# Performance work log

Hardware: AMD Instinct MI355X
Metric: run time of the kernel (lower is better)

The kernel has to match this reference:

```python
import jax, jax.numpy as jnp
import numpy as np

WS = 4        # window_size
SHIFT = 2     # shift
NHEADS = 8


def setup_inputs():
    key = jax.random.key(0)
    k = jax.random.split(key, 5)
    N, C, H, W = 16, 512, 96, 96
    x = jax.random.normal(k[0], (N, C, H, W), dtype=jnp.float32)
    # nn.MultiheadAttention parameters
    in_proj_w = jax.random.normal(k[1], (3 * C, C), dtype=jnp.float32) * 0.02
    in_proj_b = jax.random.normal(k[2], (3 * C,), dtype=jnp.float32) * 0.02
    out_w = jax.random.normal(k[3], (C, C), dtype=jnp.float32) * 0.02
    out_b = jax.random.normal(k[4], (C,), dtype=jnp.float32) * 0.02
    return {"x": x, "in_proj_w": in_proj_w, "in_proj_b": in_proj_b,
            "out_w": out_w, "out_b": out_b}


def _split_window(x, ws):
    # replicates torch: cat(split(x, ws, dim=3), dim=2); cat(split(x, ws, dim=2), dim=0)
    N, C, Hp, Wp = x.shape
    nh, nw = Hp // ws, Wp // ws
    x = x.reshape(N, C, nh, ws, nw, ws)      # n c ib wi jb wj
    x = x.transpose(4, 2, 0, 1, 3, 5)        # jb ib n c wi wj (col-block outermost in batch)
    return x.reshape(nw * nh * N, C, ws, ws), nh, nw


def _concat_window(x, nh, nw, ws):
    # inverse of _split_window, replicating torch chunk/cat order
    N = x.shape[0] // (nh * nw)
    C = x.shape[1]
    x = x.reshape(nw, nh, N, C, ws, ws)      # jb ib n c wi wj
    x = x.transpose(2, 3, 1, 4, 0, 5)        # n c ib wi jb wj
    return x.reshape(N, C, nh * ws, nw * ws)


def _mha(xt, mask_f, in_proj_w, in_proj_b, out_w, out_b):
    # xt: (B, L, C); mask_f: (B, L) FLOAT key_padding_mask -> added to logits (torch semantics)
    B, L, C = xt.shape
    d = C // NHEADS
    qkv = xt @ in_proj_w.T + in_proj_b                     # (B, L, 3C)
    q, k, v = jnp.split(qkv, 3, axis=-1)
    heads = lambda t: t.reshape(B, L, NHEADS, d).transpose(0, 2, 1, 3)  # (B, H, L, d)
    q, k, v = heads(q), heads(k), heads(v)
    scale = float(1.0 / np.sqrt(d))
    scores = jnp.einsum('bhqd,bhkd->bhqk', q, k) * scale
    scores = scores + mask_f[:, None, None, :]             # additive float key mask
    attn = jax.nn.softmax(scores, axis=-1)
    o = jnp.einsum('bhqk,bhkd->bhqd', attn, v)
    o = o.transpose(0, 2, 1, 3).reshape(B, L, C)
    return o @ out_w.T + out_b


def reference(x, in_proj_w, in_proj_b, out_w, out_b):
    N, C, H, W = x.shape
    ws = WS
    pad_h, pad_w = ws - H % ws, ws - W % ws   # note: pads a full window even when divisible
    x = jnp.pad(x, ((0, 0), (0, 0), (0, pad_h), (0, pad_w)))
    x = jnp.roll(x, (SHIFT, SHIFT), axis=(2, 3))
    # BUG-FAITHFUL: source overwrites the boolean mask with a second roll of x,
    # so the "mask" is the doubly-rolled float feature map.
    mask = jnp.roll(x, (SHIFT, SHIFT), axis=(2, 3))
    xw, nh, nw = _split_window(x, ws)
    mw, _, _ = _split_window(mask, ws)
    B = xw.shape[0]
    xt = xw.reshape(B, C, ws * ws).transpose(0, 2, 1)      # (B, L=ws*ws, C)
    mask_f = mw[:, 0].reshape(B, ws * ws)                  # channel-0 float "mask"
    ot = _mha(xt, mask_f, in_proj_w, in_proj_b, out_w, out_b)
    ow = ot.transpose(0, 2, 1).reshape(B, C, ws, ws)
    out = _concat_window(ow, nh, nw, ws)
    out = jnp.roll(out, (-SHIFT, -SHIFT), axis=(2, 3))
    return out[:, :, :H, :W]
```

## Files before the change

kernel.cpp:

```cpp
#include <hip/hip_runtime.h>
#include <cstdint>


typedef __attribute__((ext_vector_type(8))) __bf16 bf16x8;
typedef __attribute__((ext_vector_type(8))) uint16_t u16x8;
typedef __attribute__((ext_vector_type(4))) float f32x4;

__device__ __forceinline__ uint16_t f2bf(float f) {
  union { float f; uint32_t u; } c; c.f = f;
  uint32_t r = c.u + 0x7FFFu + ((c.u >> 16) & 1u);
  return (uint16_t)(r >> 16);
}
__device__ __forceinline__ float bf2f(uint16_t u) {
  union { uint32_t u; float f; } c; c.u = ((uint32_t)u) << 16;
  return c.f;
}

__device__ __forceinline__ void g2lds16(const void* g, void* lds) {
  __builtin_amdgcn_global_load_lds(
      (const __attribute__((address_space(1))) uint32_t*)(uintptr_t)g,
      (__attribute__((address_space(3))) uint32_t*)(uintptr_t)lds,
      16, 0, 0);
}

#define CFENCE asm volatile("" ::: "memory")
#define BAR do { CFENCE; __builtin_amdgcn_s_barrier(); CFENCE; } while (0)

__global__ void cvt_weights(const float* __restrict__ w1, const float* __restrict__ w2,
                            uint16_t* __restrict__ o1, uint16_t* __restrict__ o2) {
  int i = blockIdx.x * 256 + threadIdx.x;
  if (i < 786432) o1[i] = f2bf(w1[i]);
  if (i < 262144) o2[i] = f2bf(w2[i]);
}

__global__ __launch_bounds__(256) void gather_kernel(
    const float* __restrict__ x, uint16_t* __restrict__ xbf, int n0) {
  __shared__ float tile[64][65];
  const int z = blockIdx.z;
  const int g = z / 100, hh = z % 100;
  const int c0 = blockIdx.y * 64, ww0 = blockIdx.x * 64;
  const int n = n0 + g;
  const int hp = (hh >= 2) ? hh - 2 : hh + 98;
  const bool hok = hp < 96;
  const int t = threadIdx.x;
  const int lane = t & 63, grp = t >> 6;

  const int ww = ww0 + lane;
  const int wp = (ww >= 2) ? ww - 2 : ww + 98;
  const bool wok = hok && (ww < 100) && (wp < 96);
  const float* xb = x + ((size_t)n * 512) * 9216 + (size_t)hp * 96 + wp;
#pragma unroll
  for (int i = 0; i < 16; ++i) {
    int c = grp + i * 4;
    tile[c][lane] = wok ? xb[(size_t)(c0 + c) * 9216] : 0.f;
  }
  __syncthreads();
#pragma unroll
  for (int i = 0; i < 16; ++i) {
    int wl = grp + i * 4;
    int www = ww0 + wl;
    if (www < 100) {
      int m = g * 10000 + hh * 100 + www;
      xbf[(size_t)m * 512 + c0 + lane] = f2bf(tile[lane][wl]);
    }
  }
}

template <int EPI, int NB, int MODE>
__global__ __launch_bounds__(512, 2) void gemm8(
    const uint16_t* __restrict__ A, const uint16_t* __restrict__ B,
    const float* __restrict__ bias, uint16_t* __restrict__ Cbf,
    float* __restrict__ Cout, int Mg, int n0) {
  __shared__ alignas(16) uint16_t lds[65536];
  const int t = threadIdx.x;
  const int w = t >> 6, lane = t & 63;
  const int wr = w >> 2, wc = w & 3;
  const int lr = lane & 15, lg = lane >> 4;

  const int nwg = gridDim.x, bid = blockIdx.x;
  const int q = nwg >> 3, r = nwg & 7;
  const int xc = bid & 7, li = bid >> 3;
  const int wg = (xc < r ? xc * (q + 1) : r * (q + 1) + (xc - r) * q) + li;
  int bm, bn;
  if (MODE == 0) { bm = wg / NB; bn = wg % NB; }
  else           { bm = wg % NB; bn = wg / NB; }

  auto STAGE = [&](int kt, int h) {
    const uint16_t* src = (h < 2) ? A : B;
    const int row0 = ((h < 2) ? bm * 256 : bn * 256) + (h & 1) * 128;
    const int base = ((h < 2) ? 0 : 32768) + (kt & 1) * 16384 + (h & 1) * 8192;
#pragma unroll
    for (int i = 0; i < 2; ++i) {
      int e = i * 512 + t;
      int row = e >> 3, slot = e & 7;
      const uint16_t* g = src + (size_t)(row0 + row) * 512 + kt * 64 +
                          ((slot ^ (row & 7)) << 3);
      g2lds16(g, &lds[base + ((i * 512 + w * 64) << 3)]);
    }
  };
  auto LDA = [&](int cur, int mi, int k2) -> bf16x8 {
    int row = wr * 128 + mi * 16 + lr;
    int byte = cur * 32768 + row * 128 + (((k2 * 32 + lg * 8) * 2) ^ ((row & 7) << 4));
    return *(const bf16x8*)((const char*)lds + byte);
  };
  auto LDB = [&](int cur, int ni, int k2) -> bf16x8 {
    int row = wc * 64 + ni * 16 + lr;
    int byte = 65536 + cur * 32768 + row * 128 +
               (((k2 * 32 + lg * 8) * 2) ^ ((row & 7) << 4));
    return *(const bf16x8*)((const char*)lds + byte);
  };

  f32x4 acc[8][4];
#pragma unroll
  for (int mi = 0; mi < 8; ++mi)
#pragma unroll
    for (int ni = 0; ni < 4; ++ni) acc[mi][ni] = (f32x4){0.f, 0.f, 0.f, 0.f};

  STAGE(0, 0); STAGE(0, 1); STAGE(0, 2); STAGE(0, 3);
  STAGE(1, 0); STAGE(1, 1);
  asm volatile("s_waitcnt vmcnt(4)" ::: "memory");
  BAR;

#define MFMAQ(AF, BF, MIOFF, NIOFF)                                        \
  __builtin_amdgcn_s_setprio(1);                                           \
  _Pragma("unroll") for (int mi = 0; mi < 4; ++mi)                         \
  _Pragma("unroll") for (int ni = 0; ni < 2; ++ni)                         \
  _Pragma("unroll") for (int k2 = 0; k2 < 2; ++k2)                         \
      acc[mi + MIOFF][ni + NIOFF] = __builtin_amdgcn_mfma_f32_16x16x32_bf16( \
          AF[mi][k2], BF[ni][k2], acc[mi + MIOFF][ni + NIOFF], 0, 0, 0);   \
  __builtin_amdgcn_s_setprio(0);

  for (int j = 0; j < 8; ++j) {
    const int cur = j & 1;
    bf16x8 a0[4][2], a1[4][2], b0[2][2], b1[2][2];
#pragma unroll
    for (int mi = 0; mi < 4; ++mi)
#pragma unroll
      for (int k2 = 0; k2 < 2; ++k2) a0[mi][k2] = LDA(cur, mi, k2);
#pragma unroll
    for (int ni = 0; ni < 2; ++ni)
#pragma unroll
      for (int k2 = 0; k2 < 2; ++k2) b0[ni][k2] = LDB(cur, ni, k2);
    if (j + 1 < 8) STAGE(j + 1, 2);
    BAR;
    __builtin_amdgcn_sched_barrier(0);
    MFMAQ(a0, b0, 0, 0);
    BAR;
#pragma unroll
    for (int mi = 0; mi < 4; ++mi)
#pragma unroll
      for (int k2 = 0; k2 < 2; ++k2) a1[mi][k2] = LDA(cur, mi + 4, k2);
#pragma unroll
    for (int ni = 0; ni < 2; ++ni)
#pragma unroll
      for (int k2 = 0; k2 < 2; ++k2) b1[ni][k2] = LDB(cur, ni + 2, k2);
    if (j + 1 < 8) STAGE(j + 1, 3);
    BAR;
    __builtin_amdgcn_sched_barrier(0);
    MFMAQ(a1, b1, 4, 2);
    BAR;
    if (j + 2 < 8) STAGE(j + 2, 0);
    BAR;
    __builtin_amdgcn_sched_barrier(0);
    MFMAQ(a0, b1, 0, 2);
    BAR;
    if (j + 2 < 8) STAGE(j + 2, 1);
    if (j < 6) { asm volatile("s_waitcnt vmcnt(4)" ::: "memory"); }
    else       { asm volatile("s_waitcnt vmcnt(0)" ::: "memory"); }
    BAR;
    __builtin_amdgcn_sched_barrier(0);
    MFMAQ(a1, b0, 4, 0);
    BAR;
  }
#undef MFMAQ

  if (EPI == 0) {
#pragma unroll
    for (int ni = 0; ni < 4; ++ni) {
      int col = bn * 256 + wc * 64 + ni * 16 + lr;
      float bb = bias[col];
#pragma unroll
      for (int mi = 0; mi < 8; ++mi) {
        int row = bm * 256 + wr * 128 + mi * 16 + lg * 4;
#pragma unroll
        for (int rr = 0; rr < 4; ++rr)
          Cbf[(size_t)(row + rr) * 1536 + col] = f2bf(acc[mi][ni][rr] + bb);
      }
    }
  } else {
#pragma unroll
    for (int ni = 0; ni < 4; ++ni) {
      int tok = bn * 256 + wc * 64 + ni * 16 + lr;
      if (tok < Mg) {
        int g = tok / 10000, rem = tok % 10000;
        int hh = rem / 100, ww = rem % 100;
        if (hh >= 2 && hh < 98 && ww >= 2 && ww < 98) {
          size_t base = ((size_t)(n0 + g) * 512) * 9216 + (size_t)(hh - 2) * 96 + (ww - 2);
#pragma unroll
          for (int mi = 0; mi < 8; ++mi) {
            int c = bm * 256 + wr * 128 + mi * 16 + lg * 4;
#pragma unroll
            for (int rr = 0; rr < 4; ++rr)
              Cout[base + (size_t)(c + rr) * 9216] = acc[mi][ni][rr] + bias[c + rr];
          }
        }
      }
    }
  }
}

__global__ __launch_bounds__(128) void attn_kernel(
    const uint16_t* __restrict__ qkv, const float* __restrict__ x,
    uint16_t* __restrict__ obuf, int n0) {
  __shared__ alignas(16) uint16_t sq[16][1536];
  __shared__ float smask[16];
  const int b = blockIdx.x;
  const int g = b / 625, wid = b % 625;
  const int ib = wid / 25, jb = wid % 25;
  const int t = threadIdx.x;
  const int mbase = g * 10000 + ib * 400 + jb * 4;

#pragma unroll
  for (int it = 0; it < 24; ++it) {
    int e = it * 128 + t;
    int l = e / 192;
    int off = (e - l * 192) * 8;
    int m = mbase + (l >> 2) * 100 + (l & 3);
    *(uint4*)&sq[l][off] = *(const uint4*)&qkv[(size_t)m * 1536 + off];
  }
  if (t < 16) {
    int hh = ib * 4 + (t >> 2), ww = jb * 4 + (t & 3);
    int a = (hh >= 4) ? hh - 4 : hh + 96;
    int c = (ww >= 4) ? ww - 4 : ww + 96;
    smask[t] = (a < 96 && c < 96)
                   ? x[((size_t)(n0 + g) * 512) * 9216 + (size_t)a * 96 + c]
                   : 0.f;
  }
  __syncthreads();

  const int h = t >> 4, qi = t & 15;
  float qv[64];
#pragma unroll
  for (int d8 = 0; d8 < 8; ++d8) {
    u16x8 v = *(const u16x8*)&sq[qi][h * 64 + d8 * 8];
#pragma unroll
    for (int j = 0; j < 8; ++j) qv[d8 * 8 + j] = bf2f(v[j]);
  }
  float s[16];
  float mx = -1e30f;
#pragma unroll
  for (int ki = 0; ki < 16; ++ki) {
    float a = 0.f;
#pragma unroll
    for (int d8 = 0; d8 < 8; ++d8) {
      u16x8 kv = *(const u16x8*)&sq[ki][512 + h * 64 + d8 * 8];
#pragma unroll
      for (int j = 0; j < 8; ++j) a += qv[d8 * 8 + j] * bf2f(kv[j]);
    }
    s[ki] = a * 0.125f + smask[ki];
    mx = fmaxf(mx, s[ki]);
  }
  float sum = 0.f;
#pragma unroll
  for (int ki = 0; ki < 16; ++ki) { s[ki] = __expf(s[ki] - mx); sum += s[ki]; }
  const float inv = 1.f / sum;
  float o[64];
#pragma unroll
  for (int d = 0; d < 64; ++d) o[d] = 0.f;
#pragma unroll
  for (int ki = 0; ki < 16; ++ki) {
    float wgt = s[ki] * inv;
#pragma unroll
    for (int d8 = 0; d8 < 8; ++d8) {
      u16x8 vv = *(const u16x8*)&sq[ki][1024 + h * 64 + d8 * 8];
#pragma unroll
      for (int j = 0; j < 8; ++j) o[d8 * 8 + j] += wgt * bf2f(vv[j]);
    }
  }
  const int m = mbase + (qi >> 2) * 100 + (qi & 3);
#pragma unroll
  for (int d8 = 0; d8 < 8; ++d8) {
    alignas(16) uint16_t tmp[8];
#pragma unroll
    for (int j = 0; j < 8; ++j) tmp[j] = f2bf(o[d8 * 8 + j]);
    *(uint4*)&obuf[(size_t)m * 512 + h * 64 + d8 * 8] = *(uint4*)tmp;
  }
}

extern "C" void kernel_launch(void* const* d_in, const int* in_sizes, int n_in,
                              void* d_out, int out_size, void* d_ws, size_t ws_size,
                              hipStream_t stream) {
  const float* x  = (const float*)d_in[0];
  const float* wq = (const float*)d_in[1];
  const float* bq = (const float*)d_in[2];
  const float* wo = (const float*)d_in[3];
  const float* bo = (const float*)d_in[4];
  float* out = (float*)d_out;
  uint8_t* ws = (uint8_t*)d_ws;

  uint16_t* wq_bf = (uint16_t*)ws;
  uint16_t* wo_bf = (uint16_t*)(ws + 1572864);
  uint8_t* bufbase = ws + 2097152;

  int G = 16;
  while (G > 1) {
    int Mg = G * 10000;
    int Mp = ((Mg + 255) / 256) * 256;
    size_t need = (size_t)2097152 + (size_t)Mp * 4096;
    if (need <= ws_size) break;
    G >>= 1;
  }
  const int Mg = G * 10000;
  const int Mp = ((Mg + 255) / 256) * 256;
  uint16_t* xo   = (uint16_t*)bufbase;
  uint16_t* qkvb = (uint16_t*)(bufbase + (size_t)Mp * 1024);

  cvt_weights<<<dim3(3072), dim3(256), 0, stream>>>(wq, wo, wq_bf, wo_bf);

  for (int n0 = 0; n0 < 16; n0 += G) {
    gather_kernel<<<dim3(2, 8, G * 100), dim3(256), 0, stream>>>(x, xo, n0);
    gemm8<0, 6, 0><<<dim3((Mp / 256) * 6), dim3(512), 0, stream>>>(
        xo, wq_bf, bq, qkvb, nullptr, Mg, n0);
    attn_kernel<<<dim3(G * 625), dim3(128), 0, stream>>>(qkvb, x, xo, n0);
    gemm8<1, 2, 1><<<dim3((Mp / 256) * 2), dim3(512), 0, stream>>>(
        wo_bf, xo, bo, nullptr, out, Mg, n0);
  }
  (void)in_sizes; (void)n_in; (void)out_size;
}
```

Baseline: 1.063 ms.

## Reorder tokens window-major, stage GEMM epilogues through LDS, prefetch A fragments

Tokens are now laid out window-contiguous (16 tokens per window), so the attention kernel reads contiguous rows and loads K/V into LDS with direct global-to-LDS copies. Q is read straight from global memory. Both GEMM epilogues now stage results through LDS so global stores are vectorised and coalesced; the output-projection epilogue writes float2 runs into NCHW. The GEMM main loop is reordered to prefetch the next tile's A fragments early, and the MFMA operands are swapped for the QKV GEMM. The batch group size drops from 16 to 2, which adds more kernel launches but uses a smaller workspace that may stay resident in cache.

```diff
diff --git a/kernel.cpp b/kernel.cpp
--- a/kernel.cpp
+++ b/kernel.cpp
@@ -25,6 +25,7 @@
 
 #define CFENCE asm volatile("" ::: "memory")
 #define BAR do { CFENCE; __builtin_amdgcn_s_barrier(); CFENCE; } while (0)
+#define SCHED0 __builtin_amdgcn_sched_barrier(0)
 
 __global__ void cvt_weights(const float* __restrict__ w1, const float* __restrict__ w2,
                             uint16_t* __restrict__ o1, uint16_t* __restrict__ o2) {
@@ -60,7 +61,7 @@
     int wl = grp + i * 4;
     int www = ww0 + wl;
     if (www < 100) {
-      int m = g * 10000 + hh * 100 + www;
+      int m = (g * 625 + (hh >> 2) * 25 + (www >> 2)) * 16 + (hh & 3) * 4 + (www & 3);
       xbf[(size_t)m * 512 + c0 + lane] = f2bf(tile[lane][wl]);
     }
   }
@@ -93,9 +94,9 @@
     for (int i = 0; i < 2; ++i) {
       int e = i * 512 + t;
       int row = e >> 3, slot = e & 7;
-      const uint16_t* g = src + (size_t)(row0 + row) * 512 + kt * 64 +
-                          ((slot ^ (row & 7)) << 3);
-      g2lds16(g, &lds[base + ((i * 512 + w * 64) << 3)]);
+      const uint16_t* gp = src + (size_t)(row0 + row) * 512 + kt * 64 +
+                           ((slot ^ (row & 7)) << 3);
+      g2lds16(gp, &lds[base + ((i * 512 + w * 64) << 3)]);
     }
   };
   auto LDA = [&](int cur, int mi, int k2) -> bf16x8 {
@@ -109,6 +110,10 @@
                (((k2 * 32 + lg * 8) * 2) ^ ((row & 7) << 4));
     return *(const bf16x8*)((const char*)lds + byte);
   };
+  auto MM = [&](bf16x8 av, bf16x8 bv, f32x4 c) -> f32x4 {
+    if constexpr (EPI == 0) return __builtin_amdgcn_mfma_f32_16x16x32_bf16(bv, av, c, 0, 0, 0);
+    else                    return __builtin_amdgcn_mfma_f32_16x16x32_bf16(av, bv, c, 0, 0, 0);
+  };
 
   f32x4 acc[8][4];
 #pragma unroll
@@ -121,90 +126,140 @@
   asm volatile("s_waitcnt vmcnt(4)" ::: "memory");
   BAR;
 
-#define MFMAQ(AF, BF, MIOFF, NIOFF)                                        \
-  __builtin_amdgcn_s_setprio(1);                                           \
-  _Pragma("unroll") for (int mi = 0; mi < 4; ++mi)                         \
-  _Pragma("unroll") for (int ni = 0; ni < 2; ++ni)                         \
-  _Pragma("unroll") for (int k2 = 0; k2 < 2; ++k2)                         \
-      acc[mi + MIOFF][ni + NIOFF] = __builtin_amdgcn_mfma_f32_16x16x32_bf16( \
-          AF[mi][k2], BF[ni][k2], acc[mi + MIOFF][ni + NIOFF], 0, 0, 0);   \
+  bf16x8 a0[4][2], a1[4][2], b0[2][2], b1[2][2];
+#pragma unroll
+  for (int mi = 0; mi < 4; ++mi)
+#pragma unroll
+    for (int k2 = 0; k2 < 2; ++k2) a0[mi][k2] = LDA(0, mi, k2);
+
+#define MQUAD(AF, BF, MIOFF, NIOFF)                                         \
+  __builtin_amdgcn_s_setprio(1);                                            \
+  _Pragma("unroll") for (int mi = 0; mi < 4; ++mi)                          \
+  _Pragma("unroll") for (int ni = 0; ni < 2; ++ni)                          \
+  _Pragma("unroll") for (int k2 = 0; k2 < 2; ++k2)                          \
+      acc[mi + MIOFF][ni + NIOFF] =                                         \
+          MM(AF[mi][k2], BF[ni][k2], acc[mi + MIOFF][ni + NIOFF]);          \
   __builtin_amdgcn_s_setprio(0);
 
   for (int j = 0; j < 8; ++j) {
-    const int cur = j & 1;
-    bf16x8 a0[4][2], a1[4][2], b0[2][2], b1[2][2];
+    const int cur = j & 1, nxt = cur ^ 1;
+#pragma unroll
+    for (int ni = 0; ni < 2; ++ni)
+#pragma unroll
+      for (int k2 = 0; k2 < 2; ++k2) b0[ni][k2] = LDB(cur, ni, k2);
 #pragma unroll
     for (int mi = 0; mi < 4; ++mi)
 #pragma unroll
-      for (int k2 = 0; k2 < 2; ++k2) a0[mi][k2] = LDA(cur, mi, k2);
+      for (int k2 = 0; k2 < 2; ++k2) a1[mi][k2] = LDA(cur, mi + 4, k2);
 #pragma unroll
     for (int ni = 0; ni < 2; ++ni)
 #pragma unroll
-      for (int k2 = 0; k2 < 2; ++k2) b0[ni][k2] = LDB(cur, ni, k2);
+      for (int k2 = 0; k2 < 2; ++k2) b1[ni][k2] = LDB(cur, ni + 2, k2);
     if (j + 1 < 8) STAGE(j + 1, 2);
-    BAR;
-    __builtin_amdgcn_sched_barrier(0);
-    MFMAQ(a0, b0, 0, 0);
-    BAR;
-#pragma unroll
-    for (int mi = 0; mi < 4; ++mi)
-#pragma unroll
-      for (int k2 = 0; k2 < 2; ++k2) a1[mi][k2] = LDA(cur, mi + 4, k2);
-#pragma unroll
-    for (int ni = 0; ni < 2; ++ni)
-#pragma unroll
-      for (int k2 = 0; k2 < 2; ++k2) b1[ni][k2] = LDB(cur, ni + 2, k2);
+    BAR; SCHED0;
+    MQUAD(a0, b0, 0, 0);
+    BAR;
     if (j + 1 < 8) STAGE(j + 1, 3);
-    BAR;
-    __builtin_amdgcn_sched_barrier(0);
-    MFMAQ(a1, b1, 4, 2);
+    BAR; SCHED0;
+    MQUAD(a1, b1, 4, 2);
     BAR;
     if (j + 2 < 8) STAGE(j + 2, 0);
-    BAR;
-    __builtin_amdgcn_sched_barrier(0);
-    MFMAQ(a0, b1, 0, 2);
+    BAR; SCHED0;
+    MQUAD(a0, b1, 0, 2);
     BAR;
     if (j + 2 < 8) STAGE(j + 2, 1);
     if (j < 6) { asm volatile("s_waitcnt vmcnt(4)" ::: "memory"); }
     else       { asm volatile("s_waitcnt vmcnt(0)" ::: "memory"); }
     BAR;
-    __builtin_amdgcn_sched_barrier(0);
-    MFMAQ(a1, b0, 4, 0);
-    BAR;
-  }
-#undef MFMAQ
+    if (j + 1 < 8) {
+#pragma unroll
+      for (int mi = 0; mi < 4; ++mi)
+#pragma unroll
+        for (int k2 = 0; k2 < 2; ++k2) a0[mi][k2] = LDA(nxt, mi, k2);
+    }
+    SCHED0;
+    MQUAD(a1, b0, 4, 0);
+    BAR;
+  }
+#undef MQUAD
+
+  __syncthreads();
 
   if (EPI == 0) {
-#pragma unroll
-    for (int ni = 0; ni < 4; ++ni) {
-      int col = bn * 256 + wc * 64 + ni * 16 + lr;
-      float bb = bias[col];
-#pragma unroll
-      for (int mi = 0; mi < 8; ++mi) {
-        int row = bm * 256 + wr * 128 + mi * 16 + lg * 4;
-#pragma unroll
-        for (int rr = 0; rr < 4; ++rr)
-          Cbf[(size_t)(row + rr) * 1536 + col] = f2bf(acc[mi][ni][rr] + bb);
+    uint16_t* ldsE = lds;
+#pragma unroll
+    for (int p = 0; p < 2; ++p) {
+      if (wr == p) {
+#pragma unroll
+        for (int mi = 0; mi < 8; ++mi)
+#pragma unroll
+          for (int ni = 0; ni < 4; ++ni) {
+            const float* b4 = &bias[bn * 256 + wc * 64 + ni * 16 + lg * 4];
+            uint16_t pk[4];
+#pragma unroll
+            for (int rr = 0; rr < 4; ++rr) pk[rr] = f2bf(acc[mi][ni][rr] + b4[rr]);
+            uint2 v; v.x = (uint32_t)pk[0] | ((uint32_t)pk[1] << 16);
+            v.y = (uint32_t)pk[2] | ((uint32_t)pk[3] << 16);
+            *(uint2*)&ldsE[(mi * 16 + lr) * 264 + wc * 64 + ni * 16 + lg * 4] = v;
+          }
       }
+      __syncthreads();
+#pragma unroll
+      for (int i = 0; i < 8; ++i) {
+        int e = i * 512 + t;
+        int mrow = e >> 5, ch = e & 31;
+        int m = bm * 256 + p * 128 + mrow;
+        *(uint4*)&Cbf[(size_t)m * 1536 + bn * 256 + ch * 8] =
+            *(const uint4*)&ldsE[mrow * 264 + ch * 8];
+      }
+      __syncthreads();
     }
   } else {
-#pragma unroll
-    for (int ni = 0; ni < 4; ++ni) {
-      int tok = bn * 256 + wc * 64 + ni * 16 + lr;
-      if (tok < Mg) {
-        int g = tok / 10000, rem = tok % 10000;
-        int hh = rem / 100, ww = rem % 100;
-        if (hh >= 2 && hh < 98 && ww >= 2 && ww < 98) {
-          size_t base = ((size_t)(n0 + g) * 512) * 9216 + (size_t)(hh - 2) * 96 + (ww - 2);
-#pragma unroll
-          for (int mi = 0; mi < 8; ++mi) {
-            int c = bm * 256 + wr * 128 + mi * 16 + lg * 4;
+    float* ldsF = (float*)lds;
+    const int Gwin = Mg >> 4;
+#pragma unroll
+    for (int p = 0; p < 4; ++p) {
+      if (wc == p) {
+#pragma unroll
+        for (int mi = 0; mi < 8; ++mi) {
+          const float* b4 = &bias[bm * 256 + wr * 128 + mi * 16 + lg * 4];
+#pragma unroll
+          for (int ni = 0; ni < 4; ++ni)
 #pragma unroll
             for (int rr = 0; rr < 4; ++rr)
-              Cout[base + (size_t)(c + rr) * 9216] = acc[mi][ni][rr] + bias[c + rr];
+              ldsF[(wr * 128 + mi * 16 + lg * 4 + rr) * 68 + ni * 16 + lr] =
+                  acc[mi][ni][rr] + b4[rr];
+        }
+      }
+      __syncthreads();
+#pragma unroll
+      for (int i = 0; i < 8; ++i) {
+        int e = i * 512 + t;
+        int w4 = e & 3, rrow = (e >> 2) & 3, c = e >> 4;
+        int cw = bn * 16 + p * 4 + w4;
+        if (cw < Gwin) {
+          int g = cw / 625, wid = cw % 625;
+          int ib = wid / 25, jb = wid % 25;
+          int hh = ib * 4 + rrow;
+          if (hh >= 2 && hh < 98) {
+            float4 v = *(const float4*)&ldsF[c * 68 + w4 * 16 + rrow * 4];
+            size_t base = ((size_t)(n0 + g) * 512 + bm * 256 + c) * 9216 +
+                          (size_t)(hh - 2) * 96;
+            if (jb >= 1 && jb < 24) {
+              float* pp = &Cout[base + jb * 4 - 2];
+              float2 lo; lo.x = v.x; lo.y = v.y;
+              float2 hi; hi.x = v.z; hi.y = v.w;
+              *(float2*)pp = lo;
+              *(float2*)(pp + 2) = hi;
+            } else if (jb == 0) {
+              Cout[base + 0] = v.z; Cout[base + 1] = v.w;
+            } else {
+              Cout[base + 94] = v.x; Cout[base + 95] = v.y;
+            }
           }
         }
       }
+      __syncthreads();
     }
   }
 }
@@ -212,21 +267,29 @@
 __global__ __launch_bounds__(128) void attn_kernel(
     const uint16_t* __restrict__ qkv, const float* __restrict__ x,
     uint16_t* __restrict__ obuf, int n0) {
-  __shared__ alignas(16) uint16_t sq[16][1536];
+  __shared__ alignas(16) uint16_t skv[16][1024];
   __shared__ float smask[16];
   const int b = blockIdx.x;
   const int g = b / 625, wid = b % 625;
   const int ib = wid / 25, jb = wid % 25;
   const int t = threadIdx.x;
-  const int mbase = g * 10000 + ib * 400 + jb * 4;
-
-#pragma unroll
-  for (int it = 0; it < 24; ++it) {
+  const int wv = t >> 6;
+  const int mbase = b * 16;
+  const int h = t >> 4, qi = t & 15;
+
+#pragma unroll
+  for (int it = 0; it < 16; ++it) {
     int e = it * 128 + t;
-    int l = e / 192;
-    int off = (e - l * 192) * 8;
-    int m = mbase + (l >> 2) * 100 + (l & 3);
-    *(uint4*)&sq[l][off] = *(const uint4*)&qkv[(size_t)m * 1536 + off];
+    int l = e >> 7, c = e & 127;
+    const uint16_t* src = qkv + (size_t)(mbase + l) * 1536 + 512 + c * 8;
+    g2lds16(src, (uint16_t*)skv + (it * 128 + wv * 64) * 8);
+  }
+  float qv[64];
+#pragma unroll
+  for (int d8 = 0; d8 < 8; ++d8) {
+    u16x8 v = *(const u16x8*)&qkv[(size_t)(mbase + qi) * 1536 + h * 64 + d8 * 8];
+#pragma unroll
+    for (int j = 0; j < 8; ++j) qv[d8 * 8 + j] = bf2f(v[j]);
   }
   if (t < 16) {
     int hh = ib * 4 + (t >> 2), ww = jb * 4 + (t & 3);
@@ -238,14 +301,6 @@
   }
   __syncthreads();
 
-  const int h = t >> 4, qi = t & 15;
-  float qv[64];
-#pragma unroll
-  for (int d8 = 0; d8 < 8; ++d8) {
-    u16x8 v = *(const u16x8*)&sq[qi][h * 64 + d8 * 8];
-#pragma unroll
-    for (int j = 0; j < 8; ++j) qv[d8 * 8 + j] = bf2f(v[j]);
-  }
   float s[16];
   float mx = -1e30f;
 #pragma unroll
@@ -253,7 +308,7 @@
     float a = 0.f;
 #pragma unroll
     for (int d8 = 0; d8 < 8; ++d8) {
-      u16x8 kv = *(const u16x8*)&sq[ki][512 + h * 64 + d8 * 8];
+      u16x8 kv = *(const u16x8*)&skv[ki][h * 64 + d8 * 8];
 #pragma unroll
       for (int j = 0; j < 8; ++j) a += qv[d8 * 8 + j] * bf2f(kv[j]);
     }
@@ -272,12 +327,12 @@
     float wgt = s[ki] * inv;
 #pragma unroll
     for (int d8 = 0; d8 < 8; ++d8) {
-      u16x8 vv = *(const u16x8*)&sq[ki][1024 + h * 64 + d8 * 8];
+      u16x8 vv = *(const u16x8*)&skv[ki][512 + h * 64 + d8 * 8];
 #pragma unroll
       for (int j = 0; j < 8; ++j) o[d8 * 8 + j] += wgt * bf2f(vv[j]);
     }
   }
-  const int m = mbase + (qi >> 2) * 100 + (qi & 3);
+  const int m = mbase + qi;
 #pragma unroll
   for (int d8 = 0; d8 < 8; ++d8) {
     alignas(16) uint16_t tmp[8];
@@ -302,7 +357,7 @@
   uint16_t* wo_bf = (uint16_t*)(ws + 1572864);
   uint8_t* bufbase = ws + 2097152;
 
-  int G = 16;
+  int G = 2;
   while (G > 1) {
     int Mg = G * 10000;
     int Mp = ((Mg + 255) / 256) * 256;
```

After: 1.364 ms. 1.28x slower.
